# Kernel tuning notes

Measured on AMD Instinct MI355X. Metric: run time of the kernel, lower is better.

Reference implementation:

```python
import jax, jax.numpy as jnp
import numpy as np

BS = 8        # number of batched graphs (paired point clouds, must be even)
NPTS = 16384  # points per graph (equal-size graphs -> segment ops are per-row softmax)
C = 32        # feature channels
CG = 8        # global feature channels from pooling head
K = 256
KNN = 16      # key_mean_num neighbors


def setup_inputs() -> dict:
    key = jax.random.key(0)
    ks = jax.random.split(key, 5)
    N = BS * NPTS
    return {
        "feature": jax.random.normal(ks[0], (N, C, 1), dtype=jnp.float32),
        "pos": jax.random.normal(ks[1], (N, 3), dtype=jnp.float32),
        "W_pool": jax.random.normal(ks[2], (C, 1 + CG), dtype=jnp.float32) / np.float32(np.sqrt(C)),
        "W_regress": jax.random.normal(ks[3], (3 * C + 2 * CG, K), dtype=jnp.float32) / np.float32(np.sqrt(3 * C + 2 * CG)),
        "W_extract": jax.random.normal(ks[4], (C, C), dtype=jnp.float32) / np.float32(np.sqrt(C)),
        "bs": BS,
    }


def reference(feature, pos, W_pool, W_regress, W_extract, bs):
    N, Cc, _ = feature.shape
    n = N // bs
    f = feature.reshape(bs, n, Cc)          # [bs, n, C] (deg-0 fiber, D=1)
    pos_b = pos.reshape(bs, n, 3)

    # --- global pooling head: per-graph segment softmax (dgl.softmax_nodes) ---
    logits = jnp.einsum('bnc,cl->bnl', f, W_pool)      # [bs, n, 1+Cg]
    prob = jax.nn.softmax(logits[..., 0], axis=1)      # [bs, n] pooling weights
    batched = jnp.einsum('bnc,bn->bc', f, prob)        # dgl.sum_nodes weighted -> [bs, C]
    glob = jnp.einsum('bnl,bn->bl', logits[..., 1:], prob)  # [bs, Cg]

    # --- cat_0 cross-pair global merge (tensor_1 <-> tensor_2 swap) ---
    h = bs // 2
    extra = jnp.concatenate([jnp.concatenate([glob[:h], glob[h:]], 1),
                             jnp.concatenate([glob[h:], glob[:h]], 1)], 0)     # [bs, 2Cg]
    paired = jnp.concatenate([jnp.concatenate([batched[:h], batched[h:]], 1),
                              jnp.concatenate([batched[h:], batched[:h]], 1)], 0)  # [bs, 2C]
    f_new = jnp.concatenate([
        f,
        jnp.broadcast_to(extra[:, None, :], (bs, n, extra.shape[1])),   # broadcast_nodes
        jnp.broadcast_to(paired[:, None, :], (bs, n, paired.shape[1])),
    ], axis=-1)                                                          # [bs, n, 3C+2Cg]

    pw = jax.nn.softmax(jnp.einsum('bnc,ck->bnk', f_new, W_regress), axis=1)  # [bs, n, K]
    keypoints = jnp.einsum('bnk,bnd->bkd', pw, pos_b)                         # [bs, K, 3]

    # --- batched KNN: k nearest source points per keypoint, within graph ---
    d2 = jnp.sum((keypoints[:, :, None, :] - pos_b[:, None, :, :]) ** 2, axis=-1)  # [bs, K, n]
    _, idx = jax.lax.top_k(-d2, KNN)                                               # [bs, K, k]

    # --- bipartite gather + keypoint feature extraction (mean aggregate + linear) ---
    neigh = jax.vmap(lambda fb, ib: fb[ib])(f, idx)   # [bs, K, k, C]
    pooled = neigh.mean(axis=2)                        # [bs, K, C]
    return jnp.einsum('bkc,co->bko', pooled, W_extract)  # key_tensor [bs, K, C]
```

## Files before the change

kernel.cpp:

```cpp
#include <hip/hip_runtime.h>
#include <math.h>

#define BS 8
#define NPTS 16384
#define C 32
#define K 256
#define KNNK 16
#define NBINS 512
#define BININV 128.0f
#define BINW_D 0.0078125f
#define CAP 4096
#define LDSCAP 2048
#define NSPL 64

typedef float f32x4 __attribute__((ext_vector_type(4)));
typedef __bf16 bf16x8 __attribute__((ext_vector_type(8)));
union U16x8 { int4 i; bf16x8 v; unsigned short u[8]; };

__global__ __launch_bounds__(256, 2) void k_logits(
    const float* __restrict__ f, const float* __restrict__ pos,
    const float* __restrict__ Wr, float* __restrict__ partials,
    unsigned* __restrict__ ccnt) {
  int b = blockIdx.x >> 6;
  int r = blockIdx.x & 63;
  int pbase = b * NPTS + r * 256;
  int t = threadIdx.x;
  int w = t >> 6, lane = t & 63;
  int h = w & 1, nh = w >> 1;
  int quad = lane >> 4, col = lane & 15;

  if (blockIdx.x == 0 && t < BS) ccnt[t] = 0;

  __shared__ float4 posLDS[256];
  __shared__ float4 fm[2][256];

  float* rawf = (float*)&fm[0][0];
  if (t < 192) ((float4*)rawf)[t] = ((const float4*)(pos + (size_t)pbase * 3))[t];
  __syncthreads();
  float4 myp = make_float4(rawf[t * 3], rawf[t * 3 + 1], rawf[t * 3 + 2], 0.f);
  __syncthreads();
  posLDS[t] = myp;

  U16x8 Bh[8], Bl[8];
#pragma unroll
  for (int jt = 0; jt < 8; jt++) {
    int tile = h * 8 + jt;
#pragma unroll
    for (int j = 0; j < 8; j++) {
      float v = Wr[(quad * 8 + j) * K + tile * 16 + col];
      unsigned u = __float_as_uint(v);
      unsigned hb = u >> 16;
      float hf = __uint_as_float(hb << 16);
      unsigned lb = __float_as_uint(v - hf) >> 16;
      Bh[jt].u[j] = (unsigned short)hb;
      Bl[jt].u[j] = (unsigned short)lb;
    }
  }
  float acce[8], accx[8], accy[8], accz[8];
#pragma unroll
  for (int jt = 0; jt < 8; jt++) { acce[jt] = 0.f; accx[jt] = 0.f; accy[jt] = 0.f; accz[jt] = 0.f; }

#pragma unroll 1
  for (int nt = nh * 8; nt < nh * 8 + 8; nt++) {
    const float* fb = f + ((size_t)(pbase + nt * 16 + col)) * C + quad * 8;
    float4 a0 = *(const float4*)fb;
    float4 a1 = *(const float4*)(fb + 4);
    float av[8] = {a0.x, a0.y, a0.z, a0.w, a1.x, a1.y, a1.z, a1.w};
    U16x8 Ah, Al;
#pragma unroll
    for (int j = 0; j < 8; j++) {
      unsigned u = __float_as_uint(av[j]);
      unsigned hb = u >> 16;
      float hf = __uint_as_float(hb << 16);
      unsigned lb = __float_as_uint(av[j] - hf) >> 16;
      Ah.u[j] = (unsigned short)hb;
      Al.u[j] = (unsigned short)lb;
    }
    float4 pr0 = posLDS[nt * 16 + quad * 4 + 0];
    float4 pr1 = posLDS[nt * 16 + quad * 4 + 1];
    float4 pr2 = posLDS[nt * 16 + quad * 4 + 2];
    float4 pr3 = posLDS[nt * 16 + quad * 4 + 3];
#pragma unroll
    for (int jt = 0; jt < 8; jt++) {
      f32x4 d = {0.f, 0.f, 0.f, 0.f};
      d = __builtin_amdgcn_mfma_f32_16x16x32_bf16(Al.v, Bh[jt].v, d, 0, 0, 0);
      d = __builtin_amdgcn_mfma_f32_16x16x32_bf16(Ah.v, Bl[jt].v, d, 0, 0, 0);
      d = __builtin_amdgcn_mfma_f32_16x16x32_bf16(Ah.v, Bh[jt].v, d, 0, 0, 0);
      float e0 = __expf(d[0]), e1 = __expf(d[1]), e2 = __expf(d[2]), e3 = __expf(d[3]);
      acce[jt] += (e0 + e1) + (e2 + e3);
      accx[jt] += e0 * pr0.x + e1 * pr1.x + e2 * pr2.x + e3 * pr3.x;
      accy[jt] += e0 * pr0.y + e1 * pr1.y + e2 * pr2.y + e3 * pr3.y;
      accz[jt] += e0 * pr0.z + e1 * pr1.z + e2 * pr2.z + e3 * pr3.z;
    }
  }

#pragma unroll
  for (int jt = 0; jt < 8; jt++) {
    acce[jt] += __shfl_xor(acce[jt], 16); acce[jt] += __shfl_xor(acce[jt], 32);
    accx[jt] += __shfl_xor(accx[jt], 16); accx[jt] += __shfl_xor(accx[jt], 32);
    accy[jt] += __shfl_xor(accy[jt], 16); accy[jt] += __shfl_xor(accy[jt], 32);
    accz[jt] += __shfl_xor(accz[jt], 16); accz[jt] += __shfl_xor(accz[jt], 32);
  }
  __syncthreads();
  if (lane < 16) {
#pragma unroll
    for (int jt = 0; jt < 8; jt++)
      fm[nh][h * 128 + jt * 16 + lane] = make_float4(acce[jt], accx[jt], accy[jt], accz[jt]);
  }
  __syncthreads();
  float4 v0 = fm[0][t], v1 = fm[1][t];
  float4* po = (float4*)partials;
  po[(size_t)blockIdx.x * 256 + t] =
      make_float4(v0.x + v1.x, v0.y + v1.y, v0.z + v1.z, v0.w + v1.w);
}

__global__ __launch_bounds__(256) void k_cand(
    const float* __restrict__ pos, const float* __restrict__ partials,
    float* __restrict__ kpts, unsigned* __restrict__ ccnt,
    float4* __restrict__ cand) {
  int g = blockIdx.x >> 3;
  int ch = blockIdx.x & 7;
  int t = threadIdx.x;
  int lane = t & 63, wave = t >> 6;

  __shared__ float kxs[256], kys[256], kzs[256];
  __shared__ float wred[4][4];
  __shared__ float bc[4];
  __shared__ unsigned hist[NBINS];
  __shared__ unsigned sc[NBINS];
  __shared__ int mbin;
  __shared__ unsigned lcnt, gbase;
  __shared__ float cxs[2048], cys[2048], czs[2048];
  __shared__ int cis[2048];

  hist[t] = 0; hist[t + 256] = 0;
  if (t == 0) { lcnt = 0; mbin = NBINS - 1; }

  {
    const float4* po = (const float4*)partials;
    float L = 0.f, X = 0.f, Y = 0.f, Z = 0.f;
#pragma unroll 8
    for (int s = 0; s < NSPL; s++) {
      float4 v = po[((size_t)(g * NSPL + s)) * 256 + t];
      L += v.x; X += v.y; Y += v.z; Z += v.w;
    }
    float inv = 1.f / L;
    float kx = X * inv, ky = Y * inv, kz = Z * inv;
    kxs[t] = kx; kys[t] = ky; kzs[t] = kz;
    if (ch == 0) ((float4*)kpts)[g * 256 + t] = make_float4(kx, ky, kz, 0.f);
  }
  __syncthreads();

  float sx = kxs[t], sy = kys[t], sz = kzs[t];
#pragma unroll
  for (int off = 32; off; off >>= 1) {
    sx += __shfl_xor(sx, off, 64);
    sy += __shfl_xor(sy, off, 64);
    sz += __shfl_xor(sz, off, 64);
  }
  if (lane == 0) { wred[wave][0] = sx; wred[wave][1] = sy; wred[wave][2] = sz; }
  __syncthreads();
  if (t == 0) {
    float X = 0.f, Y = 0.f, Z = 0.f;
#pragma unroll
    for (int i = 0; i < 4; i++) { X += wred[i][0]; Y += wred[i][1]; Z += wred[i][2]; }
    bc[0] = X / K; bc[1] = Y / K; bc[2] = Z / K;
  }
  __syncthreads();
  float cx = bc[0], cy = bc[1], cz = bc[2];

  {
    float dx = kxs[t] - cx, dy = kys[t] - cy, dz = kzs[t] - cz;
    float md = dx * dx + dy * dy + dz * dz;
#pragma unroll
    for (int off = 32; off; off >>= 1) md = fmaxf(md, __shfl_xor(md, off, 64));
    if (lane == 0) wred[wave][3] = md;
  }
  __syncthreads();
  if (t == 0) {
    float m = fmaxf(fmaxf(wred[0][3], wred[1][3]), fmaxf(wred[2][3], wred[3][3]));
    bc[3] = sqrtf(m);
  }
  __syncthreads();
  float maxd = bc[3];

  float pxr[8], pyr[8], pzr[8], pdr[8];
#pragma unroll
  for (int i = 0; i < 8; i++) {
    int pl = ch * 2048 + i * 256 + t;
    const float* pp = pos + (size_t)(g * NPTS + pl) * 3;
    pxr[i] = pp[0]; pyr[i] = pp[1]; pzr[i] = pp[2];
    float dx = pxr[i] - cx, dy = pyr[i] - cy, dz = pzr[i] - cz;
    pdr[i] = dx * dx + dy * dy + dz * dz;
    int bin = (int)(sqrtf(pdr[i]) * BININV);
    if (bin < NBINS - 1) atomicAdd(&hist[bin], 1u);
  }
  __syncthreads();

  sc[t] = hist[t]; sc[t + 256] = hist[t + 256];
  __syncthreads();
  for (int off = 1; off < NBINS; off <<= 1) {
    unsigned a0 = (t >= off) ? sc[t - off] : 0u;
    unsigned a1 = ((t + 256) >= off) ? sc[t + 256 - off] : 0u;
    __syncthreads();
    sc[t] += a0; sc[t + 256] += a1;
    __syncthreads();
  }
  {
    unsigned c0 = sc[t], p0 = t ? sc[t - 1] : 0u;
    unsigned c1 = sc[t + 256], p1 = sc[t + 255];
    if (c0 >= KNNK && p0 < KNNK) atomicMin(&mbin, t);
    if ((t + 256) < (NBINS - 1) && c1 >= KNNK && p1 < KNNK) atomicMin(&mbin, t + 256);
  }
  __syncthreads();
  float r2;
  if (mbin < NBINS - 1) {
    float Rf = (mbin + 1) * BINW_D + 2.f * maxd;
    r2 = Rf * Rf;
  } else r2 = 3.0e38f;

#pragma unroll
  for (int i = 0; i < 8; i++) {
    if (pdr[i] <= r2) {
      unsigned u = atomicAdd(&lcnt, 1u);
      cxs[u] = pxr[i]; cys[u] = pyr[i]; czs[u] = pzr[i];
      cis[u] = ch * 2048 + i * 256 + t;
    }
  }
  __syncthreads();
  if (t == 0) gbase = atomicAdd(&ccnt[g], lcnt);
  __syncthreads();
  unsigned nl = lcnt, base = gbase;
  for (unsigned j = t; j < nl; j += 256) {
    unsigned dst = base + j;
    if (dst < CAP)
      cand[(size_t)g * CAP + dst] = make_float4(cxs[j], cys[j], czs[j], __int_as_float(cis[j]));
  }
}

__global__ __launch_bounds__(256) void k_topk_ext(
    const float* __restrict__ pos, const float* __restrict__ f,
    const float* __restrict__ We, const float* __restrict__ kpts,
    const unsigned* __restrict__ ccnt, const float4* __restrict__ cand,
    float* __restrict__ out) {
  int g = blockIdx.x >> 3;
  int sb = blockIdx.x & 7;
  int t = threadIdx.x;
  int kp = t >> 3;
  int part = t & 7;

  __shared__ float cxs[LDSCAP], cys[LDSCAP], czs[LDSCAP];
  __shared__ int cis[LDSCAP];
  __shared__ int nidx[32][KNNK];
  __shared__ float P[8][C + 1];
  __shared__ float WeL[C][C + 1];

  unsigned cnt = ccnt[g];
  int ovf = cnt > LDSCAP;
  int n = ovf ? 0 : (int)cnt;
  for (int j = t; j < n; j += 256) {
    float4 v = cand[(size_t)g * CAP + j];
    cxs[j] = v.x; cys[j] = v.y; czs[j] = v.z; cis[j] = __float_as_int(v.w);
  }
#pragma unroll
  for (int i = 0; i < 4; i++) {
    int idx = t + i * 256;
    WeL[idx >> 5][idx & 31] = We[idx];
  }
  __syncthreads();

  float4 kpt = ((const float4*)kpts)[g * 256 + sb * 32 + kp];
  float kx = kpt.x, ky = kpt.y, kz = kpt.z;
  float dd[KNNK]; int ii[KNNK];
#pragma unroll
  for (int j = 0; j < KNNK; j++) { dd[j] = 1e30f; ii[j] = 0; }
  float mx = 1e30f;

  if (!ovf) {
    for (int j = part; j < n; j += 8) {
      float dx = kx - cxs[j], dy = ky - cys[j], dz = kz - czs[j];
      float d2 = dx * dx + dy * dy + dz * dz;
      if (d2 < mx) {
        int sm = 0; float bv = dd[0];
#pragma unroll
        for (int s = 1; s < KNNK; s++) if (dd[s] > bv) { bv = dd[s]; sm = s; }
#pragma unroll
        for (int s = 0; s < KNNK; s++) if (s == sm) { dd[s] = d2; ii[s] = j; }
        mx = dd[0];
#pragma unroll
        for (int s = 1; s < KNNK; s++) mx = fmaxf(mx, dd[s]);
      }
    }
  } else {
    for (int j = part; j < NPTS; j += 8) {
      const float* pp = pos + (size_t)(g * NPTS + j) * 3;
      float dx = kx - pp[0], dy = ky - pp[1], dz = kz - pp[2];
      float d2 = dx * dx + dy * dy + dz * dz;
      if (d2 < mx) {
        int sm = 0; float bv = dd[0];
#pragma unroll
        for (int s = 1; s < KNNK; s++) if (dd[s] > bv) { bv = dd[s]; sm = s; }
#pragma unroll
        for (int s = 0; s < KNNK; s++) if (s == sm) { dd[s] = d2; ii[s] = j; }
        mx = dd[0];
#pragma unroll
        for (int s = 1; s < KNNK; s++) mx = fmaxf(mx, dd[s]);
      }
    }
  }

#pragma unroll 1
  for (int r = 0; r < KNNK; r++) {
    float bv = dd[0]; int sm = 0;
#pragma unroll
    for (int s = 1; s < KNNK; s++) if (dd[s] < bv) { bv = dd[s]; sm = s; }
    int bi = 0;
#pragma unroll
    for (int s = 0; s < KNNK; s++) if (s == sm) bi = ii[s];
    unsigned khi = __float_as_uint(bv), klo = (unsigned)bi;
    unsigned whi = khi, wlo = klo;
#pragma unroll
    for (int off = 1; off < 8; off <<= 1) {
      unsigned h2 = __shfl_xor(whi, off, 64);
      unsigned l2 = __shfl_xor(wlo, off, 64);
      if (h2 < whi || (h2 == whi && l2 < wlo)) { whi = h2; wlo = l2; }
    }
    if (whi == khi && wlo == klo) {
#pragma unroll
      for (int s = 0; s < KNNK; s++) if (s == sm) dd[s] = 1e30f;
    }
    if (part == 0) {
      int jw = (int)wlo;
      nidx[kp][r] = ovf ? jw : cis[jw];
    }
  }
  __syncthreads();

  int c = t & 31, kl = t >> 5;
#pragma unroll 1
  for (int hh = 0; hh < 4; hh++) {
    int kk = hh * 8 + kl;
    float s = 0.f;
#pragma unroll
    for (int j = 0; j < KNNK; j++) {
      int pl = nidx[kk][j];
      s += f[((size_t)(g * NPTS + pl)) * C + c];
    }
    P[kl][c] = s * (1.f / KNNK);
    __syncthreads();
    float r = 0.f;
#pragma unroll
    for (int cc = 0; cc < C; cc++) r += P[kl][cc] * WeL[cc][c];
    out[((size_t)(g * K + sb * 32 + kk)) * C + c] = r;
    __syncthreads();
  }
}

extern "C" void kernel_launch(void* const* d_in, const int* in_sizes, int n_in,
                              void* d_out, int out_size, void* d_ws, size_t ws_size,
                              hipStream_t stream) {
  const float* f   = (const float*)d_in[0];
  const float* pos = (const float*)d_in[1];
  const float* Wr  = (const float*)d_in[3];
  const float* We  = (const float*)d_in[4];
  float* out = (float*)d_out;

  char* ws = (char*)d_ws;
  float*    partials = (float*)(ws + 0);
  float*    kpts     = (float*)(ws + 2097152);
  unsigned* ccnt     = (unsigned*)(ws + 2129920);
  float4*   cand     = (float4*)(ws + 2130432);

  k_logits  <<<dim3(BS * NSPL), dim3(256), 0, stream>>>(f, pos, Wr, partials, ccnt);
  k_cand    <<<dim3(BS * 8),    dim3(256), 0, stream>>>(pos, partials, kpts, ccnt, cand);
  k_topk_ext<<<dim3(BS * 8),    dim3(256), 0, stream>>>(pos, f, We, kpts, ccnt, cand, out);
}
```

Baseline: 122.9 us.

## Fuse candidate selection into top-k kernel, recomputing per-graph histogram redundantly

Merges the candidate-filter kernel and the top-k/extract kernel into one launch. Each of the eight blocks per graph now scans all 16384 points of its graph to build the histogram and gather candidates straight into LDS. This removes the global candidate buffer, the atomic counter, the keypoint round trip and one kernel launch. The cost is that each block does eight times the point-scanning and histogram work, and the points are read from global memory twice.

After: 141.4 us. +15.0%, slower.

```diff
diff --git a/kernel.cpp b/kernel.cpp
--- a/kernel.cpp
+++ b/kernel.cpp
@@ -9,7 +9,6 @@
 #define NBINS 512
 #define BININV 128.0f
 #define BINW_D 0.0078125f
-#define CAP 4096
 #define LDSCAP 2048
 #define NSPL 64
 
@@ -19,8 +18,7 @@
 
 __global__ __launch_bounds__(256, 2) void k_logits(
     const float* __restrict__ f, const float* __restrict__ pos,
-    const float* __restrict__ Wr, float* __restrict__ partials,
-    unsigned* __restrict__ ccnt) {
+    const float* __restrict__ Wr, float* __restrict__ partials) {
   int b = blockIdx.x >> 6;
   int r = blockIdx.x & 63;
   int pbase = b * NPTS + r * 256;
@@ -28,8 +26,6 @@
   int w = t >> 6, lane = t & 63;
   int h = w & 1, nh = w >> 1;
   int quad = lane >> 4, col = lane & 15;
-
-  if (blockIdx.x == 0 && t < BS) ccnt[t] = 0;
 
   __shared__ float4 posLDS[256];
   __shared__ float4 fm[2][256];
@@ -114,12 +110,12 @@
       make_float4(v0.x + v1.x, v0.y + v1.y, v0.z + v1.z, v0.w + v1.w);
 }
 
-__global__ __launch_bounds__(256) void k_cand(
-    const float* __restrict__ pos, const float* __restrict__ partials,
-    float* __restrict__ kpts, unsigned* __restrict__ ccnt,
-    float4* __restrict__ cand) {
+__global__ __launch_bounds__(256) void k_sel(
+    const float* __restrict__ pos, const float* __restrict__ f,
+    const float* __restrict__ We, const float* __restrict__ partials,
+    float* __restrict__ out) {
   int g = blockIdx.x >> 3;
-  int ch = blockIdx.x & 7;
+  int sb = blockIdx.x & 7;
   int t = threadIdx.x;
   int lane = t & 63, wave = t >> 6;
 
@@ -129,12 +125,20 @@
   __shared__ unsigned hist[NBINS];
   __shared__ unsigned sc[NBINS];
   __shared__ int mbin;
-  __shared__ unsigned lcnt, gbase;
-  __shared__ float cxs[2048], cys[2048], czs[2048];
-  __shared__ int cis[2048];
+  __shared__ unsigned lcnt;
+  __shared__ float cxs[LDSCAP], cys[LDSCAP], czs[LDSCAP];
+  __shared__ int cis[LDSCAP];
+  __shared__ int nidx[32][KNNK];
+  __shared__ float P[8][C + 1];
+  __shared__ float WeL[C][C + 1];
 
   hist[t] = 0; hist[t + 256] = 0;
   if (t == 0) { lcnt = 0; mbin = NBINS - 1; }
+#pragma unroll
+  for (int i = 0; i < 4; i++) {
+    int idx = t + i * 256;
+    WeL[idx >> 5][idx & 31] = We[idx];
+  }
 
   {
     const float4* po = (const float4*)partials;
@@ -145,9 +149,7 @@
       L += v.x; X += v.y; Y += v.z; Z += v.w;
     }
     float inv = 1.f / L;
-    float kx = X * inv, ky = Y * inv, kz = Z * inv;
-    kxs[t] = kx; kys[t] = ky; kzs[t] = kz;
-    if (ch == 0) ((float4*)kpts)[g * 256 + t] = make_float4(kx, ky, kz, 0.f);
+    kxs[t] = X * inv; kys[t] = Y * inv; kzs[t] = Z * inv;
   }
   __syncthreads();
 
@@ -184,15 +186,12 @@
   __syncthreads();
   float maxd = bc[3];
 
-  float pxr[8], pyr[8], pzr[8], pdr[8];
-#pragma unroll
-  for (int i = 0; i < 8; i++) {
-    int pl = ch * 2048 + i * 256 + t;
-    const float* pp = pos + (size_t)(g * NPTS + pl) * 3;
-    pxr[i] = pp[0]; pyr[i] = pp[1]; pzr[i] = pp[2];
-    float dx = pxr[i] - cx, dy = pyr[i] - cy, dz = pzr[i] - cz;
-    pdr[i] = dx * dx + dy * dy + dz * dz;
-    int bin = (int)(sqrtf(pdr[i]) * BININV);
+#pragma unroll 4
+  for (int i = 0; i < 64; i++) {
+    const float* pp = pos + (size_t)(g * NPTS + i * 256 + t) * 3;
+    float dx = pp[0] - cx, dy = pp[1] - cy, dz = pp[2] - cz;
+    float d2 = dx * dx + dy * dy + dz * dz;
+    int bin = (int)(sqrtf(d2) * BININV);
     if (bin < NBINS - 1) atomicAdd(&hist[bin], 1u);
   }
   __syncthreads();
@@ -219,58 +218,27 @@
     r2 = Rf * Rf;
   } else r2 = 3.0e38f;
 
-#pragma unroll
-  for (int i = 0; i < 8; i++) {
-    if (pdr[i] <= r2) {
+#pragma unroll 4
+  for (int i = 0; i < 64; i++) {
+    int pl = i * 256 + t;
+    const float* pp = pos + (size_t)(g * NPTS + pl) * 3;
+    float px = pp[0], py = pp[1], pz = pp[2];
+    float dx = px - cx, dy = py - cy, dz = pz - cz;
+    float d2 = dx * dx + dy * dy + dz * dz;
+    if (d2 <= r2) {
       unsigned u = atomicAdd(&lcnt, 1u);
-      cxs[u] = pxr[i]; cys[u] = pyr[i]; czs[u] = pzr[i];
-      cis[u] = ch * 2048 + i * 256 + t;
-    }
-  }
-  __syncthreads();
-  if (t == 0) gbase = atomicAdd(&ccnt[g], lcnt);
-  __syncthreads();
-  unsigned nl = lcnt, base = gbase;
-  for (unsigned j = t; j < nl; j += 256) {
-    unsigned dst = base + j;
-    if (dst < CAP)
-      cand[(size_t)g * CAP + dst] = make_float4(cxs[j], cys[j], czs[j], __int_as_float(cis[j]));
-  }
-}
-
-__global__ __launch_bounds__(256) void k_topk_ext(
-    const float* __restrict__ pos, const float* __restrict__ f,
-    const float* __restrict__ We, const float* __restrict__ kpts,
-    const unsigned* __restrict__ ccnt, const float4* __restrict__ cand,
-    float* __restrict__ out) {
-  int g = blockIdx.x >> 3;
-  int sb = blockIdx.x & 7;
-  int t = threadIdx.x;
+      if (u < LDSCAP) { cxs[u] = px; cys[u] = py; czs[u] = pz; cis[u] = pl; }
+    }
+  }
+  __syncthreads();
+
+  unsigned cnt = lcnt;
+  int ovf = cnt > LDSCAP;
+  int n = ovf ? 0 : (int)cnt;
+
   int kp = t >> 3;
   int part = t & 7;
-
-  __shared__ float cxs[LDSCAP], cys[LDSCAP], czs[LDSCAP];
-  __shared__ int cis[LDSCAP];
-  __shared__ int nidx[32][KNNK];
-  __shared__ float P[8][C + 1];
-  __shared__ float WeL[C][C + 1];
-
-  unsigned cnt = ccnt[g];
-  int ovf = cnt > LDSCAP;
-  int n = ovf ? 0 : (int)cnt;
-  for (int j = t; j < n; j += 256) {
-    float4 v = cand[(size_t)g * CAP + j];
-    cxs[j] = v.x; cys[j] = v.y; czs[j] = v.z; cis[j] = __float_as_int(v.w);
-  }
-#pragma unroll
-  for (int i = 0; i < 4; i++) {
-    int idx = t + i * 256;
-    WeL[idx >> 5][idx & 31] = We[idx];
-  }
-  __syncthreads();
-
-  float4 kpt = ((const float4*)kpts)[g * 256 + sb * 32 + kp];
-  float kx = kpt.x, ky = kpt.y, kz = kpt.z;
+  float kx = kxs[sb * 32 + kp], ky = kys[sb * 32 + kp], kz = kzs[sb * 32 + kp];
   float dd[KNNK]; int ii[KNNK];
 #pragma unroll
   for (int j = 0; j < KNNK; j++) { dd[j] = 1e30f; ii[j] = 0; }
@@ -365,13 +333,8 @@
   const float* We  = (const float*)d_in[4];
   float* out = (float*)d_out;
 
-  char* ws = (char*)d_ws;
-  float*    partials = (float*)(ws + 0);
-  float*    kpts     = (float*)(ws + 2097152);
-  unsigned* ccnt     = (unsigned*)(ws + 2129920);
-  float4*   cand     = (float4*)(ws + 2130432);
-
-  k_logits  <<<dim3(BS * NSPL), dim3(256), 0, stream>>>(f, pos, Wr, partials, ccnt);
-  k_cand    <<<dim3(BS * 8),    dim3(256), 0, stream>>>(pos, partials, kpts, ccnt, cand);
-  k_topk_ext<<<dim3(BS * 8),    dim3(256), 0, stream>>>(pos, f, We, kpts, ccnt, cand, out);
+  float* partials = (float*)d_ws;
+
+  k_logits<<<dim3(BS * NSPL), dim3(256), 0, stream>>>(f, pos, Wr, partials);
+  k_sel   <<<dim3(BS * 8),    dim3(256), 0, stream>>>(pos, f, We, partials, out);
 }
```
